# Performance work log

Hardware: AMD Instinct MI355X
Metric: run time of the kernel (lower is better)

## Reference

```python
import jax, jax.numpy as jnp
import numpy as np

M, K, E = 4096, 7168, 2048  # tokens, hidden_size, expert_dim

def setup_inputs() -> dict:
    key = jax.random.key(0)
    k1, k2, k3 = jax.random.split(key, 3)
    x = jax.random.normal(k1, (M, K), dtype=jnp.float32)
    # NT layout: weights stored [n, k]
    w_up_gate = jax.random.normal(k2, (2 * E, K), dtype=jnp.float32) * (1.0 / np.sqrt(K))
    w_down = jax.random.normal(k3, (K, E), dtype=jnp.float32) * (1.0 / np.sqrt(E))
    return {"x": x, "w_up_gate": w_up_gate, "w_down": w_down}

def reference(x, w_up_gate, w_down):
    # up_gate GEMM: [m, k] @ [n, k]^T -> [m, 2*E]
    ug = jnp.einsum('mk,nk->mn', x, w_up_gate)
    gate, up = jnp.split(ug, 2, axis=-1)          # each [m, E]
    h = jax.nn.silu(gate) * up                     # SwiGLU activation
    # down GEMM: [m, E] @ [hidden, E]^T -> [m, hidden]
    out = jnp.einsum('me,he->mh', h, w_down)
    return out
```

## Files before the change

kernel.cpp:

```cpp
#include <hip/hip_runtime.h>
#include <hip/hip_bf16.h>
#include <stdint.h>

typedef __attribute__((ext_vector_type(8))) short     bf16x8;
typedef __attribute__((ext_vector_type(4))) float     f32x4;
typedef __attribute__((ext_vector_type(8))) unsigned short u16x8;

__device__ __forceinline__ unsigned short f2bf(float f) {
  unsigned int u = __float_as_uint(f);
  u += 0x7FFFu + ((u >> 16) & 1u);
  return (unsigned short)(u >> 16);
}
__device__ __forceinline__ float bf2f(unsigned short s) {
  return __uint_as_float(((unsigned int)s) << 16);
}

__device__ __forceinline__ void async_cp16(const void* g, void* l) {
  __builtin_amdgcn_global_load_lds((const __attribute__((address_space(1))) void*)g,
                                   (__attribute__((address_space(3))) void*)l,
                                   16, 0, 0);
}

__global__ __launch_bounds__(256) void cvt_f32_to_bf16(const float* __restrict__ in,
                                                       unsigned short* __restrict__ out,
                                                       int n4) {
  int i = blockIdx.x * blockDim.x + threadIdx.x;
  const int stride = gridDim.x * blockDim.x;
  for (; i < n4; i += stride) {
    const float4 v = ((const float4*)in)[i];
    ushort4 o;
    o.x = f2bf(v.x); o.y = f2bf(v.y); o.z = f2bf(v.z); o.w = f2bf(v.w);
    ((ushort4*)out)[i] = o;
  }
}

__global__ __launch_bounds__(256) void swiglu_k(const unsigned short* __restrict__ ug,
                                                unsigned short* __restrict__ h,
                                                int total8) {
  int i = blockIdx.x * blockDim.x + threadIdx.x;
  const int stride = gridDim.x * blockDim.x;
  for (; i < total8; i += stride) {
    const int m = i >> 8;
    const int e = (i & 255) << 3;
    const u16x8 g = *(const u16x8*)(ug + (size_t)m * 4096 + e);
    const u16x8 u = *(const u16x8*)(ug + (size_t)m * 4096 + 2048 + e);
    u16x8 o;
#pragma unroll
    for (int j = 0; j < 8; ++j) {
      const float gv = bf2f((unsigned short)g[j]);
      const float uv = bf2f((unsigned short)u[j]);
      const float s  = gv / (1.0f + __expf(-gv));
      o[j] = f2bf(s * uv);
    }
    *(u16x8*)(h + (size_t)m * 2048 + e) = o;
  }
}

template <int K, int N, bool OUT_BF16>
__global__ __launch_bounds__(512, 2) void gemm_nt(const unsigned short* __restrict__ A,
                                                  const unsigned short* __restrict__ B,
                                                  void* __restrict__ Cv) {
  extern __shared__ char sm[];
  constexpr int nbx = N / 256;
  constexpr int nwg = (4096 / 256) * nbx;
  constexpr size_t K2 = (size_t)K * 2;

  const int bid = blockIdx.x;
  constexpr int q8 = nwg / 8;
  const int swz = (bid & 7) * q8 + (bid >> 3);
  const int bx = swz % nbx, by = swz / nbx;
  const int row0 = by * 256, col0 = bx * 256;

  const int tid = threadIdx.x, wave = tid >> 6, lane = tid & 63;
  const int wr = wave >> 2, wc = wave & 3;
  const int fr = lane & 15, fg = lane >> 4;

  const int l3 = lane >> 3;
  const int q  = (lane & 7) ^ l3;
  const int qr = q >> 2;
  const int qc = (q & 3) * 16;
  const char* gA[2]; const char* gB[2];
#pragma unroll
  for (int i = 0; i < 2; ++i) {
    const int L = i * 64 + wave * 8 + l3;
    gA[i] = (const char*)A + (size_t)(row0 + 2 * L + qr) * K2 + qc;
    gB[i] = (const char*)B + (size_t)(col0 + 2 * L + qr) * K2 + qc;
  }

  const int rbA = wr * 128 + fr;
  const int offA0 = (rbA >> 1) * 128 + (((((rbA & 1) << 2) | fg) ^ ((rbA >> 1) & 7)) << 4);
  const int rbB = wc * 64 + fr;
  const int offB0 = (rbB >> 1) * 128 + (((((rbB & 1) << 2) | fg) ^ ((rbB >> 1) & 7)) << 4);

  f32x4 acc[8][4];
#pragma unroll
  for (int m = 0; m < 8; ++m)
#pragma unroll
    for (int n = 0; n < 4; ++n) acc[m][n] = (f32x4){0.f, 0.f, 0.f, 0.f};

  constexpr int nh = K / 32;

#define STAGE_A(h, slot) do {                                   \
    char* d_ = sm + (slot) * 16384 + wave * 1024;               \
    async_cp16(gA[0] + (size_t)(h) * 64, d_);                   \
    async_cp16(gA[1] + (size_t)(h) * 64, d_ + 8192);            \
  } while (0)
#define STAGE_B(h, slot) do {                                   \
    char* d_ = sm + 65536 + (slot) * 16384 + wave * 1024;       \
    async_cp16(gB[0] + (size_t)(h) * 64, d_);                   \
    async_cp16(gB[1] + (size_t)(h) * 64, d_ + 8192);            \
  } while (0)

#pragma unroll
  for (int hp = 0; hp < 3; ++hp) { STAGE_A(hp, hp); STAGE_B(hp, hp); }

  for (int h = 0; h < nh; ++h) {
    const int slot = h & 3;
    asm volatile("s_waitcnt vmcnt(8)" ::: "memory");
    __builtin_amdgcn_s_barrier();

    const char* aBase = sm + slot * 16384;
    const char* bBase = sm + 65536 + slot * 16384;
    const int hs = (h + 3 < nh) ? h + 3 : nh - 1;
    const int sslot = (h + 3) & 3;

    bf16x8 af[4], bfr[4];
#pragma unroll
    for (int n = 0; n < 4; ++n) bfr[n] = *(const bf16x8*)(bBase + offB0 + n * 1024);
#pragma unroll
    for (int m = 0; m < 4; ++m) af[m] = *(const bf16x8*)(aBase + offA0 + m * 1024);
    STAGE_A(hs, sslot);
    __builtin_amdgcn_s_barrier();
    __builtin_amdgcn_s_setprio(1);
#pragma unroll
    for (int m = 0; m < 4; ++m)
#pragma unroll
      for (int n = 0; n < 4; ++n)
        acc[m][n] = __builtin_amdgcn_mfma_f32_16x16x32_bf16(af[m], bfr[n], acc[m][n], 0, 0, 0);
    __builtin_amdgcn_s_setprio(0);
    __builtin_amdgcn_s_barrier();

#pragma unroll
    for (int m = 0; m < 4; ++m) af[m] = *(const bf16x8*)(aBase + offA0 + (m + 4) * 1024);
    STAGE_B(hs, sslot);
    __builtin_amdgcn_s_barrier();
    __builtin_amdgcn_s_setprio(1);
#pragma unroll
    for (int m = 0; m < 4; ++m)
#pragma unroll
      for (int n = 0; n < 4; ++n)
        acc[m + 4][n] = __builtin_amdgcn_mfma_f32_16x16x32_bf16(af[m], bfr[n], acc[m + 4][n], 0, 0, 0);
    __builtin_amdgcn_s_setprio(0);
    __builtin_amdgcn_s_barrier();
  }
#undef STAGE_A
#undef STAGE_B

  const int rowb = row0 + wr * 128 + fg * 4;
  const int colb = col0 + wc * 64 + fr;
  if (OUT_BF16) {
    unsigned short* Cp = (unsigned short*)Cv;
#pragma unroll
    for (int m = 0; m < 8; ++m)
#pragma unroll
      for (int n = 0; n < 4; ++n)
#pragma unroll
        for (int j = 0; j < 4; ++j)
          Cp[(size_t)(rowb + m * 16 + j) * N + (colb + n * 16)] = f2bf(acc[m][n][j]);
  } else {
    float* Cp = (float*)Cv;
#pragma unroll
    for (int m = 0; m < 8; ++m)
#pragma unroll
      for (int n = 0; n < 4; ++n)
#pragma unroll
        for (int j = 0; j < 4; ++j)
          Cp[(size_t)(rowb + m * 16 + j) * N + (colb + n * 16)] = acc[m][n][j];
  }
}

extern "C" void kernel_launch(void* const* d_in, const int* in_sizes, int n_in,
                              void* d_out, int out_size, void* d_ws, size_t ws_size,
                              hipStream_t stream) {
  const int M = 4096, K = 7168, E = 2048;

  const float* x   = (const float*)d_in[0];
  const float* wug = (const float*)d_in[1];
  const float* wd  = (const float*)d_in[2];
  float* out = (float*)d_out;

  char* ws = (char*)d_ws;
  unsigned short* xb  = (unsigned short*)(ws);
  unsigned short* wub = (unsigned short*)(ws + 58720256);
  unsigned short* wdb = (unsigned short*)(ws + 117440512);
  unsigned short* ug  = (unsigned short*)(ws + 146800640);
  unsigned short* h   = (unsigned short*)(ws + 180355072);
  if (ws_size < 197132288) return;

  hipFuncSetAttribute((const void*)gemm_nt<7168, 4096, true>,
                      hipFuncAttributeMaxDynamicSharedMemorySize, 131072);
  hipFuncSetAttribute((const void*)gemm_nt<2048, 7168, false>,
                      hipFuncAttributeMaxDynamicSharedMemorySize, 131072);

  cvt_f32_to_bf16<<<2048, 256, 0, stream>>>(x,   xb,  M * K / 4);
  cvt_f32_to_bf16<<<2048, 256, 0, stream>>>(wug, wub, 2 * E * K / 4);
  cvt_f32_to_bf16<<<1024, 256, 0, stream>>>(wd,  wdb, K * E / 4);

  gemm_nt<7168, 4096, true><<<256, 512, 131072, stream>>>(xb, wub, ug);

  swiglu_k<<<2048, 256, 0, stream>>>(ug, h, M * E / 8);

  gemm_nt<2048, 7168, false><<<448, 512, 131072, stream>>>(h, wdb, out);
}
```

Baseline: 407.4 us.

## Fuse SwiGLU into up-gate GEMM epilogue via permuted weights; trim barriers

The up/gate weight rows are permuted during bf16 conversion so each 32-row group interleaves 16 gate rows with their 16 matching up rows. This puts gate and up values for the same column in one wave's accumulators, so the GEMM epilogue computes silu(gate)*up and writes h directly. That removes the separate SwiGLU kernel and the round trip of the full ug intermediate through memory. The main loop also drops from four barriers per K step to one, relying on the 4-slot ring with prefetch distance 3 to avoid read/write races on shared memory. This trades fewer synchronisations for less scheduling control between waves.

```diff
diff --git a/kernel.cpp b/kernel.cpp
--- a/kernel.cpp
+++ b/kernel.cpp
@@ -4,15 +4,11 @@
 
 typedef __attribute__((ext_vector_type(8))) short     bf16x8;
 typedef __attribute__((ext_vector_type(4))) float     f32x4;
-typedef __attribute__((ext_vector_type(8))) unsigned short u16x8;
 
 __device__ __forceinline__ unsigned short f2bf(float f) {
   unsigned int u = __float_as_uint(f);
   u += 0x7FFFu + ((u >> 16) & 1u);
   return (unsigned short)(u >> 16);
-}
-__device__ __forceinline__ float bf2f(unsigned short s) {
-  return __uint_as_float(((unsigned int)s) << 16);
 }
 
 __device__ __forceinline__ void async_cp16(const void* g, void* l) {
@@ -34,29 +30,23 @@
   }
 }
 
-__global__ __launch_bounds__(256) void swiglu_k(const unsigned short* __restrict__ ug,
-                                                unsigned short* __restrict__ h,
-                                                int total8) {
+__global__ __launch_bounds__(256) void cvt_wug_perm(const float* __restrict__ in,
+                                                    unsigned short* __restrict__ out,
+                                                    int n4) {
   int i = blockIdx.x * blockDim.x + threadIdx.x;
   const int stride = gridDim.x * blockDim.x;
-  for (; i < total8; i += stride) {
-    const int m = i >> 8;
-    const int e = (i & 255) << 3;
-    const u16x8 g = *(const u16x8*)(ug + (size_t)m * 4096 + e);
-    const u16x8 u = *(const u16x8*)(ug + (size_t)m * 4096 + 2048 + e);
-    u16x8 o;
-#pragma unroll
-    for (int j = 0; j < 8; ++j) {
-      const float gv = bf2f((unsigned short)g[j]);
-      const float uv = bf2f((unsigned short)u[j]);
-      const float s  = gv / (1.0f + __expf(-gv));
-      o[j] = f2bf(s * uv);
-    }
-    *(u16x8*)(h + (size_t)m * 2048 + e) = o;
-  }
-}
-
-template <int K, int N, bool OUT_BF16>
+  for (; i < n4; i += stride) {
+    const int r = i / 1792, c = i - r * 1792;
+    const int g = r >> 5, w = r & 31;
+    const int src = g * 16 + (w & 15) + ((w & 16) ? 2048 : 0);
+    const float4 v = ((const float4*)in)[(size_t)src * 1792 + c];
+    ushort4 o;
+    o.x = f2bf(v.x); o.y = f2bf(v.y); o.z = f2bf(v.z); o.w = f2bf(v.w);
+    ((ushort4*)out)[(size_t)r * 1792 + c] = o;
+  }
+}
+
+template <int K, int N, bool FUSE_SWIGLU>
 __global__ __launch_bounds__(512, 2) void gemm_nt(const unsigned short* __restrict__ A,
                                                   const unsigned short* __restrict__ B,
                                                   void* __restrict__ Cv) {
@@ -113,12 +103,11 @@
 
 #pragma unroll
   for (int hp = 0; hp < 3; ++hp) { STAGE_A(hp, hp); STAGE_B(hp, hp); }
+  asm volatile("s_waitcnt vmcnt(8)" ::: "memory");
+  __builtin_amdgcn_s_barrier();
 
   for (int h = 0; h < nh; ++h) {
     const int slot = h & 3;
-    asm volatile("s_waitcnt vmcnt(8)" ::: "memory");
-    __builtin_amdgcn_s_barrier();
-
     const char* aBase = sm + slot * 16384;
     const char* bBase = sm + 65536 + slot * 16384;
     const int hs = (h + 3 < nh) ? h + 3 : nh - 1;
@@ -130,7 +119,6 @@
 #pragma unroll
     for (int m = 0; m < 4; ++m) af[m] = *(const bf16x8*)(aBase + offA0 + m * 1024);
     STAGE_A(hs, sslot);
-    __builtin_amdgcn_s_barrier();
     __builtin_amdgcn_s_setprio(1);
 #pragma unroll
     for (int m = 0; m < 4; ++m)
@@ -138,12 +126,10 @@
       for (int n = 0; n < 4; ++n)
         acc[m][n] = __builtin_amdgcn_mfma_f32_16x16x32_bf16(af[m], bfr[n], acc[m][n], 0, 0, 0);
     __builtin_amdgcn_s_setprio(0);
-    __builtin_amdgcn_s_barrier();
 
 #pragma unroll
     for (int m = 0; m < 4; ++m) af[m] = *(const bf16x8*)(aBase + offA0 + (m + 4) * 1024);
     STAGE_B(hs, sslot);
-    __builtin_amdgcn_s_barrier();
     __builtin_amdgcn_s_setprio(1);
 #pragma unroll
     for (int m = 0; m < 4; ++m)
@@ -151,24 +137,31 @@
       for (int n = 0; n < 4; ++n)
         acc[m + 4][n] = __builtin_amdgcn_mfma_f32_16x16x32_bf16(af[m], bfr[n], acc[m + 4][n], 0, 0, 0);
     __builtin_amdgcn_s_setprio(0);
+
+    asm volatile("s_waitcnt vmcnt(8)" ::: "memory");
     __builtin_amdgcn_s_barrier();
   }
 #undef STAGE_A
 #undef STAGE_B
 
   const int rowb = row0 + wr * 128 + fg * 4;
-  const int colb = col0 + wc * 64 + fr;
-  if (OUT_BF16) {
-    unsigned short* Cp = (unsigned short*)Cv;
+  if (FUSE_SWIGLU) {
+    unsigned short* Hp = (unsigned short*)Cv;
+    const int ecb = ((col0 + wc * 64) >> 1) + fr;
 #pragma unroll
     for (int m = 0; m < 8; ++m)
 #pragma unroll
-      for (int n = 0; n < 4; ++n)
-#pragma unroll
-        for (int j = 0; j < 4; ++j)
-          Cp[(size_t)(rowb + m * 16 + j) * N + (colb + n * 16)] = f2bf(acc[m][n][j]);
+      for (int p = 0; p < 2; ++p)
+#pragma unroll
+        for (int j = 0; j < 4; ++j) {
+          const float gv = acc[m][2 * p][j];
+          const float uv = acc[m][2 * p + 1][j];
+          const float s  = gv / (1.0f + __expf(-gv));
+          Hp[(size_t)(rowb + m * 16 + j) * (N / 2) + (ecb + p * 16)] = f2bf(s * uv);
+        }
   } else {
     float* Cp = (float*)Cv;
+    const int colb = col0 + wc * 64 + fr;
 #pragma unroll
     for (int m = 0; m < 8; ++m)
 #pragma unroll
@@ -193,9 +186,8 @@
   unsigned short* xb  = (unsigned short*)(ws);
   unsigned short* wub = (unsigned short*)(ws + 58720256);
   unsigned short* wdb = (unsigned short*)(ws + 117440512);
-  unsigned short* ug  = (unsigned short*)(ws + 146800640);
-  unsigned short* h   = (unsigned short*)(ws + 180355072);
-  if (ws_size < 197132288) return;
+  unsigned short* h   = (unsigned short*)(ws + 146800640);
+  if (ws_size < 163577856) return;
 
   hipFuncSetAttribute((const void*)gemm_nt<7168, 4096, true>,
                       hipFuncAttributeMaxDynamicSharedMemorySize, 131072);
@@ -203,12 +195,10 @@
                       hipFuncAttributeMaxDynamicSharedMemorySize, 131072);
 
   cvt_f32_to_bf16<<<2048, 256, 0, stream>>>(x,   xb,  M * K / 4);
-  cvt_f32_to_bf16<<<2048, 256, 0, stream>>>(wug, wub, 2 * E * K / 4);
+  cvt_wug_perm  <<<2048, 256, 0, stream>>>(wug, wub, 2 * E * K / 4);
   cvt_f32_to_bf16<<<1024, 256, 0, stream>>>(wd,  wdb, K * E / 4);
 
-  gemm_nt<7168, 4096, true><<<256, 512, 131072, stream>>>(xb, wub, ug);
-
-  swiglu_k<<<2048, 256, 0, stream>>>(ug, h, M * E / 8);
+  gemm_nt<7168, 4096, true><<<256, 512, 131072, stream>>>(xb, wub, h);
 
   gemm_nt<2048, 7168, false><<<448, 512, 131072, stream>>>(h, wdb, out);
 }
```

After: 388.9 us. -4.5%, faster.
